# Performance work log

Measured on AMD Instinct MI355X. Metric: run time of the kernel, lower is better.

Reference implementation:

```python
import jax, jax.numpy as jnp
import numpy as np

B, F, D, A = 1024, 33, 128, 128  # batch, num_fields, embed_dim, attn_size (A must equal gnn dim)

def setup_inputs() -> dict:
    key = jax.random.key(0)
    k1, k2, k3, k4 = jax.random.split(key, 4)
    gnn_feature = jax.random.normal(k1, (B, A), dtype=jnp.float32)
    x = jax.random.normal(k2, (B, F, D), dtype=jnp.float32)
    # attention Linear(embed_dim -> attn_size): weight (A, D), bias (A,)
    lim = 1.0 / np.sqrt(D)
    attn_W = jax.random.uniform(k3, (A, D), minval=-lim, maxval=lim, dtype=jnp.float32)
    attn_b = jax.random.uniform(k4, (A,), minval=-lim, maxval=lim, dtype=jnp.float32)
    return {"gnn_feature": gnn_feature, "x": x, "attn_W": attn_W, "attn_b": attn_b}

def reference(gnn_feature, x, attn_W, attn_b):
    num_fields = x.shape[1]
    row, col = np.triu_indices(num_fields, k=1)  # P = F*(F-1)/2 pairs
    inner = x[:, row] * x[:, col]                # [B, P, D]
    fm = jax.nn.relu(jnp.einsum('bpd,ad->bpa', inner, attn_W) + attn_b)  # [B, P, A]
    # bmm(gnn[b,1,A], fm[b,p,A,1]) -> dot product per pair, softmax over pairs
    scores = jnp.einsum('ba,bpa->bp', gnn_feature, fm)  # [B, P]
    attn = jax.nn.softmax(scores, axis=1)               # [B, P]
    attn_output = jnp.einsum('bp,bpd->bd', attn, inner) * 100.0  # [B, D]
    return jnp.concatenate([gnn_feature, attn_output], axis=1)   # [B, A+D]
```

## Files before the change

### kernel.cpp

```cpp
#include <hip/hip_runtime.h>

#define FN 33
#define DN 128
#define AN 128
#define PN 528
#define XS 136
#define TS 36

typedef __attribute__((ext_vector_type(8))) _Float16 half8;
typedef __attribute__((ext_vector_type(4))) float f32x4;
typedef __attribute__((ext_vector_type(4))) unsigned int u32x4;

__device__ __forceinline__ unsigned int pkrtz(float a, float b) {
  return __builtin_bit_cast(unsigned int, __builtin_amdgcn_cvt_pkrtz(a, b));
}

__device__ __forceinline__ float row_sum16(float v) {
  v += __builtin_bit_cast(float, __builtin_amdgcn_update_dpp(0, __builtin_bit_cast(int, v), 0x128, 0xF, 0xF, false));
  v += __builtin_bit_cast(float, __builtin_amdgcn_update_dpp(0, __builtin_bit_cast(int, v), 0x124, 0xF, 0xF, false));
  v += __builtin_bit_cast(float, __builtin_amdgcn_update_dpp(0, __builtin_bit_cast(int, v), 0x122, 0xF, 0xF, false));
  v += __builtin_bit_cast(float, __builtin_amdgcn_update_dpp(0, __builtin_bit_cast(int, v), 0x121, 0xF, 0xF, false));
  return v;
}

__global__ __launch_bounds__(256, 4)
void afm_kernel(const float* __restrict__ gnn, const float* __restrict__ xg,
                const float* __restrict__ Wg,  const float* __restrict__ bg,
                float* __restrict__ out)
{
  __shared__ __align__(16) _Float16 xh[FN * XS];
  __shared__ __align__(16) float attn2d[FN * TS];
  __shared__ __align__(16) float sp[2][PN];
  __shared__ __align__(16) float part[256];
  __shared__ unsigned short rowcol[PN];
  __shared__ float red[8];

  const int tid  = threadIdx.x;
  const int b    = blockIdx.x;
  const int wave = tid >> 6;
  const int lane = tid & 63;
  const int q    = lane >> 4;
  const int u    = lane & 15;
  const int nh   = wave & 1;
  const int mh   = wave >> 1;

  half8 Bf[4][4];
  float garr[4], barr[4];
  #pragma unroll
  for (int nn = 0; nn < 4; nn++) {
    const int a = (nh * 4 + nn) * 16 + u;
    const float* src = Wg + (size_t)a * DN + q * 8;
    #pragma unroll
    for (int kk = 0; kk < 4; kk++) {
      f32x4 w0 = *(const f32x4*)(src + kk * 32);
      f32x4 w1 = *(const f32x4*)(src + kk * 32 + 4);
      u32x4 pk;
      pk.x = pkrtz(w0.x, w0.y);
      pk.y = pkrtz(w0.z, w0.w);
      pk.z = pkrtz(w1.x, w1.y);
      pk.w = pkrtz(w1.z, w1.w);
      Bf[nn][kk] = __builtin_bit_cast(half8, pk);
      asm volatile("" : "+v"(Bf[nn][kk]));
    }
    garr[nn] = gnn[(size_t)b * AN + a];
    barr[nn] = bg[a];
    asm volatile("" : "+v"(garr[nn]), "+v"(barr[nn]));
  }

  for (int idx = tid; idx < FN * TS; idx += 256) attn2d[idx] = 0.0f;

  const f32x4* xg4 = (const f32x4*)(xg + (size_t)b * FN * DN);
  for (int idx = tid; idx < (FN * DN) / 4; idx += 256) {
    f32x4 v = xg4[idx];
    int i  = idx >> 5;
    int d0 = (idx & 31) << 2;
    *(uint2*)&xh[i * XS + d0] = make_uint2(pkrtz(v.x, v.y), pkrtz(v.z, v.w));
  }
  for (int p = tid; p < PN; p += 256) {
    int i = 0, rem = p;
    while (rem >= FN - 1 - i) { rem -= FN - 1 - i; i++; }
    rowcol[p] = (unsigned short)(i | ((i + 1 + rem) << 8));
  }
  __syncthreads();

  const int mt_beg = mh ? 17 : 0;
  const int mt_end = mh ? 33 : 17;
  unsigned int rc_next = rowcol[mt_beg * 16 + u];
  for (int mt = mt_beg; mt < mt_end; ++mt) {
    const unsigned int rc = rc_next;
    if (mt + 1 < mt_end) rc_next = rowcol[(mt + 1) * 16 + u];
    const int r = rc & 255, c = rc >> 8;
    const _Float16* xr_base = &xh[r * XS + q * 8];
    const _Float16* xc_base = &xh[c * XS + q * 8];

    f32x4 acc[4];
    #pragma unroll
    for (int nn = 0; nn < 4; nn++) acc[nn] = (f32x4){0.f, 0.f, 0.f, 0.f};

    #pragma unroll
    for (int kk = 0; kk < 4; kk++) {
      half8 xr = *(const half8*)(xr_base + kk * 32);
      half8 xc = *(const half8*)(xc_base + kk * 32);
      half8 af = xr * xc;
      #pragma unroll
      for (int nn = 0; nn < 4; nn++)
        acc[nn] = __builtin_amdgcn_mfma_f32_16x16x32_f16(af, Bf[nn][kk], acc[nn], 0, 0, 0);
    }

    float sc[4] = {0.f, 0.f, 0.f, 0.f};
    #pragma unroll
    for (int nn = 0; nn < 4; nn++)
      #pragma unroll
      for (int rr = 0; rr < 4; rr++) {
        float fmv = fmaxf(acc[nn][rr] + barr[nn], 0.f);
        sc[rr] = fmaf(fmv, garr[nn], sc[rr]);
      }
    #pragma unroll
    for (int rr = 0; rr < 4; rr++) sc[rr] = row_sum16(sc[rr]);
    if (u == 0)
      *(f32x4*)&sp[nh][mt * 16 + q * 4] = (f32x4){sc[0], sc[1], sc[2], sc[3]};
  }
  __syncthreads();

  float s0 = sp[0][tid] + sp[1][tid];
  float s1 = sp[0][tid + 256] + sp[1][tid + 256];
  float s2 = (tid < 16) ? (sp[0][tid + 512] + sp[1][tid + 512]) : -3.4e38f;
  float m = fmaxf(fmaxf(s0, s1), s2);
  #pragma unroll
  for (int off = 32; off >= 1; off >>= 1) m = fmaxf(m, __shfl_xor(m, off, 64));
  if (lane == 0) red[wave] = m;
  __syncthreads();
  const float smax = fmaxf(fmaxf(red[0], red[1]), fmaxf(red[2], red[3]));

  float e0 = __expf(s0 - smax);
  float e1 = __expf(s1 - smax);
  float e2 = (tid < 16) ? __expf(s2 - smax) : 0.f;
  {
    unsigned int rc = rowcol[tid];
    attn2d[(rc & 255) * TS + ((rc >> 8) - (rc & 255) - 1)] = e0;
    rc = rowcol[tid + 256];
    attn2d[(rc & 255) * TS + ((rc >> 8) - (rc & 255) - 1)] = e1;
    if (tid < 16) {
      rc = rowcol[tid + 512];
      attn2d[(rc & 255) * TS + ((rc >> 8) - (rc & 255) - 1)] = e2;
    }
  }
  float lsum = e0 + e1 + e2;
  #pragma unroll
  for (int off = 32; off >= 1; off >>= 1) lsum += __shfl_xor(lsum, off, 64);
  if (lane == 0) red[4 + wave] = lsum;
  __syncthreads();
  const float Z = red[4] + red[5] + red[6] + red[7];

  {
    const int d = tid & 127;
    const int h = tid >> 7;
    float xcol[36];
    #pragma unroll
    for (int i = 0; i < FN; i++) xcol[i] = (float)xh[i * XS + d];
    xcol[33] = 0.f; xcol[34] = 0.f; xcol[35] = 0.f;

    float acc = 0.f;
    #pragma unroll
    for (int i = 0; i < 32; i++) {
      if ((i & 1) != h) continue;
      const int L = FN - 1 - i;
      const int nf4 = (L + 3) >> 2;
      float ti = 0.f;
      #pragma unroll
      for (int t = 0; t < nf4; t++) {
        f32x4 a4 = *(const f32x4*)&attn2d[i * TS + t * 4];
        ti = fmaf(a4.x, xcol[i + 1 + t * 4 + 0], ti);
        ti = fmaf(a4.y, xcol[i + 1 + t * 4 + 1], ti);
        ti = fmaf(a4.z, xcol[i + 1 + t * 4 + 2], ti);
        ti = fmaf(a4.w, xcol[i + 1 + t * 4 + 3], ti);
      }
      acc = fmaf(xcol[i], ti, acc);
    }
    part[tid] = acc;
  }
  __syncthreads();
  if (tid < DN) {
    float tot = part[tid] + part[tid + 128];
    out[(size_t)b * (AN + DN) + AN + tid] = tot * (100.0f / Z);
  } else {
    const int a = tid - 128;
    out[(size_t)b * (AN + DN) + a] = gnn[(size_t)b * AN + a];
  }
}

extern "C" void kernel_launch(void* const* d_in, const int* in_sizes, int n_in,
                              void* d_out, int out_size, void* d_ws, size_t ws_size,
                              hipStream_t stream) {
  (void)n_in; (void)out_size; (void)d_ws; (void)ws_size;
  const float* gnn  = (const float*)d_in[0];
  const float* x    = (const float*)d_in[1];
  const float* W    = (const float*)d_in[2];
  const float* bias = (const float*)d_in[3];
  float* out = (float*)d_out;
  const int Bn = in_sizes[0] / AN;
  afm_kernel<<<dim3(Bn), dim3(256), 0, stream>>>(gnn, x, W, bias, out);
}
```

Before: 112.6 us.

## Split attention N dimension four ways across waves, each wave covering all pair tiles

```diff
diff --git a/kernel.cpp b/kernel.cpp
--- a/kernel.cpp
+++ b/kernel.cpp
@@ -30,7 +30,7 @@
 {
   __shared__ __align__(16) _Float16 xh[FN * XS];
   __shared__ __align__(16) float attn2d[FN * TS];
-  __shared__ __align__(16) float sp[2][PN];
+  __shared__ __align__(16) float sp[4][PN];
   __shared__ __align__(16) float part[256];
   __shared__ unsigned short rowcol[PN];
   __shared__ float red[8];
@@ -41,14 +41,13 @@
   const int lane = tid & 63;
   const int q    = lane >> 4;
   const int u    = lane & 15;
-  const int nh   = wave & 1;
-  const int mh   = wave >> 1;
-
-  half8 Bf[4][4];
-  float garr[4], barr[4];
+  const int nq   = wave;
+
+  half8 Bf[2][4];
+  float garr[2], barr[2];
   #pragma unroll
-  for (int nn = 0; nn < 4; nn++) {
-    const int a = (nh * 4 + nn) * 16 + u;
+  for (int nn = 0; nn < 2; nn++) {
+    const int a = nq * 32 + nn * 16 + u;
     const float* src = Wg + (size_t)a * DN + q * 8;
     #pragma unroll
     for (int kk = 0; kk < 4; kk++) {
@@ -83,48 +82,93 @@
   }
   __syncthreads();
 
-  const int mt_beg = mh ? 17 : 0;
-  const int mt_end = mh ? 33 : 17;
-  unsigned int rc_next = rowcol[mt_beg * 16 + u];
-  for (int mt = mt_beg; mt < mt_end; ++mt) {
-    const unsigned int rc = rc_next;
-    if (mt + 1 < mt_end) rc_next = rowcol[(mt + 1) * 16 + u];
-    const int r = rc & 255, c = rc >> 8;
-    const _Float16* xr_base = &xh[r * XS + q * 8];
-    const _Float16* xc_base = &xh[c * XS + q * 8];
-
-    f32x4 acc[4];
-    #pragma unroll
-    for (int nn = 0; nn < 4; nn++) acc[nn] = (f32x4){0.f, 0.f, 0.f, 0.f};
-
+  unsigned int rc0 = rowcol[u];
+  unsigned int rc1 = rowcol[16 + u];
+  for (int t = 0; t < 16; ++t) {
+    const int r0 = rc0 & 255, c0 = rc0 >> 8;
+    const int r1 = rc1 & 255, c1 = rc1 >> 8;
+    const _Float16* xr0 = &xh[r0 * XS + q * 8];
+    const _Float16* xc0 = &xh[c0 * XS + q * 8];
+    const _Float16* xr1 = &xh[r1 * XS + q * 8];
+    const _Float16* xc1 = &xh[c1 * XS + q * 8];
+    if (t < 15) {
+      rc0 = rowcol[(t + 1) * 32 + u];
+      rc1 = rowcol[(t + 1) * 32 + 16 + u];
+    } else {
+      rc0 = rowcol[512 + u];
+    }
+
+    f32x4 acc0[2], acc1[2];
+    #pragma unroll
+    for (int nn = 0; nn < 2; nn++) {
+      acc0[nn] = (f32x4){0.f, 0.f, 0.f, 0.f};
+      acc1[nn] = (f32x4){0.f, 0.f, 0.f, 0.f};
+    }
+
+    __builtin_amdgcn_s_setprio(1);
     #pragma unroll
     for (int kk = 0; kk < 4; kk++) {
-      half8 xr = *(const half8*)(xr_base + kk * 32);
-      half8 xc = *(const half8*)(xc_base + kk * 32);
-      half8 af = xr * xc;
-      #pragma unroll
-      for (int nn = 0; nn < 4; nn++)
-        acc[nn] = __builtin_amdgcn_mfma_f32_16x16x32_f16(af, Bf[nn][kk], acc[nn], 0, 0, 0);
-    }
-
-    float sc[4] = {0.f, 0.f, 0.f, 0.f};
-    #pragma unroll
-    for (int nn = 0; nn < 4; nn++)
+      half8 a0 = *(const half8*)(xr0 + kk * 32) * *(const half8*)(xc0 + kk * 32);
+      half8 a1 = *(const half8*)(xr1 + kk * 32) * *(const half8*)(xc1 + kk * 32);
+      acc0[0] = __builtin_amdgcn_mfma_f32_16x16x32_f16(a0, Bf[0][kk], acc0[0], 0, 0, 0);
+      acc1[0] = __builtin_amdgcn_mfma_f32_16x16x32_f16(a1, Bf[0][kk], acc1[0], 0, 0, 0);
+      acc0[1] = __builtin_amdgcn_mfma_f32_16x16x32_f16(a0, Bf[1][kk], acc0[1], 0, 0, 0);
+      acc1[1] = __builtin_amdgcn_mfma_f32_16x16x32_f16(a1, Bf[1][kk], acc1[1], 0, 0, 0);
+    }
+    __builtin_amdgcn_s_setprio(0);
+
+    float sc0[4] = {0.f, 0.f, 0.f, 0.f};
+    float sc1[4] = {0.f, 0.f, 0.f, 0.f};
+    #pragma unroll
+    for (int nn = 0; nn < 2; nn++)
       #pragma unroll
       for (int rr = 0; rr < 4; rr++) {
-        float fmv = fmaxf(acc[nn][rr] + barr[nn], 0.f);
-        sc[rr] = fmaf(fmv, garr[nn], sc[rr]);
+        sc0[rr] = fmaf(fmaxf(acc0[nn][rr] + barr[nn], 0.f), garr[nn], sc0[rr]);
+        sc1[rr] = fmaf(fmaxf(acc1[nn][rr] + barr[nn], 0.f), garr[nn], sc1[rr]);
       }
     #pragma unroll
-    for (int rr = 0; rr < 4; rr++) sc[rr] = row_sum16(sc[rr]);
+    for (int rr = 0; rr < 4; rr++) {
+      sc0[rr] = row_sum16(sc0[rr]);
+      sc1[rr] = row_sum16(sc1[rr]);
+    }
+    if (u == 0) {
+      *(f32x4*)&sp[nq][t * 32 + q * 4]      = (f32x4){sc0[0], sc0[1], sc0[2], sc0[3]};
+      *(f32x4*)&sp[nq][t * 32 + 16 + q * 4] = (f32x4){sc1[0], sc1[1], sc1[2], sc1[3]};
+    }
+  }
+  {
+    const int r0 = rc0 & 255, c0 = rc0 >> 8;
+    const _Float16* xr0 = &xh[r0 * XS + q * 8];
+    const _Float16* xc0 = &xh[c0 * XS + q * 8];
+    f32x4 acc0[2];
+    acc0[0] = (f32x4){0.f, 0.f, 0.f, 0.f};
+    acc0[1] = (f32x4){0.f, 0.f, 0.f, 0.f};
+    __builtin_amdgcn_s_setprio(1);
+    #pragma unroll
+    for (int kk = 0; kk < 4; kk++) {
+      half8 a0 = *(const half8*)(xr0 + kk * 32) * *(const half8*)(xc0 + kk * 32);
+      acc0[0] = __builtin_amdgcn_mfma_f32_16x16x32_f16(a0, Bf[0][kk], acc0[0], 0, 0, 0);
+      acc0[1] = __builtin_amdgcn_mfma_f32_16x16x32_f16(a0, Bf[1][kk], acc0[1], 0, 0, 0);
+    }
+    __builtin_amdgcn_s_setprio(0);
+    float sc0[4] = {0.f, 0.f, 0.f, 0.f};
+    #pragma unroll
+    for (int nn = 0; nn < 2; nn++)
+      #pragma unroll
+      for (int rr = 0; rr < 4; rr++)
+        sc0[rr] = fmaf(fmaxf(acc0[nn][rr] + barr[nn], 0.f), garr[nn], sc0[rr]);
+    #pragma unroll
+    for (int rr = 0; rr < 4; rr++) sc0[rr] = row_sum16(sc0[rr]);
     if (u == 0)
-      *(f32x4*)&sp[nh][mt * 16 + q * 4] = (f32x4){sc[0], sc[1], sc[2], sc[3]};
-  }
-  __syncthreads();
-
-  float s0 = sp[0][tid] + sp[1][tid];
-  float s1 = sp[0][tid + 256] + sp[1][tid + 256];
-  float s2 = (tid < 16) ? (sp[0][tid + 512] + sp[1][tid + 512]) : -3.4e38f;
+      *(f32x4*)&sp[nq][512 + q * 4] = (f32x4){sc0[0], sc0[1], sc0[2], sc0[3]};
+  }
+  __syncthreads();
+
+  float s0 = (sp[0][tid] + sp[1][tid]) + (sp[2][tid] + sp[3][tid]);
+  float s1 = (sp[0][tid + 256] + sp[1][tid + 256]) + (sp[2][tid + 256] + sp[3][tid + 256]);
+  float s2 = (tid < 16)
+           ? ((sp[0][tid + 512] + sp[1][tid + 512]) + (sp[2][tid + 512] + sp[3][tid + 512]))
+           : -3.4e38f;
   float m = fmaxf(fmaxf(s0, s1), s2);
   #pragma unroll
   for (int off = 32; off >= 1; off >>= 1) m = fmaxf(m, __shfl_xor(m, off, 64));
```

New measurement: 110.9 us. Within noise of the previous version (-1.5%).

## Double block size to 512 threads, splitting pair tiles across four wave pairs

Applied to the files above, without the earlier changes.

```diff
diff --git a/kernel.cpp b/kernel.cpp
--- a/kernel.cpp
+++ b/kernel.cpp
@@ -23,7 +23,7 @@
   return v;
 }
 
-__global__ __launch_bounds__(256, 4)
+__global__ __launch_bounds__(512, 4)
 void afm_kernel(const float* __restrict__ gnn, const float* __restrict__ xg,
                 const float* __restrict__ Wg,  const float* __restrict__ bg,
                 float* __restrict__ out)
@@ -31,9 +31,9 @@
   __shared__ __align__(16) _Float16 xh[FN * XS];
   __shared__ __align__(16) float attn2d[FN * TS];
   __shared__ __align__(16) float sp[2][PN];
-  __shared__ __align__(16) float part[256];
+  __shared__ __align__(16) float part[512];
   __shared__ unsigned short rowcol[PN];
-  __shared__ float red[8];
+  __shared__ float red[16];
 
   const int tid  = threadIdx.x;
   const int b    = blockIdx.x;
@@ -42,13 +42,13 @@
   const int q    = lane >> 4;
   const int u    = lane & 15;
   const int nh   = wave & 1;
-  const int mh   = wave >> 1;
+  const int mq   = wave >> 1;
 
   half8 Bf[4][4];
   float garr[4], barr[4];
   #pragma unroll
   for (int nn = 0; nn < 4; nn++) {
-    const int a = (nh * 4 + nn) * 16 + u;
+    const int a = nh * 64 + nn * 16 + u;
     const float* src = Wg + (size_t)a * DN + q * 8;
     #pragma unroll
     for (int kk = 0; kk < 4; kk++) {
@@ -67,28 +67,28 @@
     asm volatile("" : "+v"(garr[nn]), "+v"(barr[nn]));
   }
 
-  for (int idx = tid; idx < FN * TS; idx += 256) attn2d[idx] = 0.0f;
+  for (int idx = tid; idx < FN * TS; idx += 512) attn2d[idx] = 0.0f;
 
   const f32x4* xg4 = (const f32x4*)(xg + (size_t)b * FN * DN);
-  for (int idx = tid; idx < (FN * DN) / 4; idx += 256) {
+  for (int idx = tid; idx < (FN * DN) / 4; idx += 512) {
     f32x4 v = xg4[idx];
     int i  = idx >> 5;
     int d0 = (idx & 31) << 2;
     *(uint2*)&xh[i * XS + d0] = make_uint2(pkrtz(v.x, v.y), pkrtz(v.z, v.w));
   }
-  for (int p = tid; p < PN; p += 256) {
+  for (int p = tid; p < PN; p += 512) {
     int i = 0, rem = p;
     while (rem >= FN - 1 - i) { rem -= FN - 1 - i; i++; }
     rowcol[p] = (unsigned short)(i | ((i + 1 + rem) << 8));
   }
   __syncthreads();
 
-  const int mt_beg = mh ? 17 : 0;
-  const int mt_end = mh ? 33 : 17;
-  unsigned int rc_next = rowcol[mt_beg * 16 + u];
-  for (int mt = mt_beg; mt < mt_end; ++mt) {
+  const int t_beg = (mq == 0) ? 0 : (mq * 8 + 1);
+  const int t_end = (mq + 1) * 8 + 1;
+  unsigned int rc_next = rowcol[t_beg * 16 + u];
+  for (int t = t_beg; t < t_end; ++t) {
     const unsigned int rc = rc_next;
-    if (mt + 1 < mt_end) rc_next = rowcol[(mt + 1) * 16 + u];
+    if (t + 1 < t_end) rc_next = rowcol[(t + 1) * 16 + u];
     const int r = rc & 255, c = rc >> 8;
     const _Float16* xr_base = &xh[r * XS + q * 8];
     const _Float16* xc_base = &xh[c * XS + q * 8];
@@ -97,64 +97,62 @@
     #pragma unroll
     for (int nn = 0; nn < 4; nn++) acc[nn] = (f32x4){0.f, 0.f, 0.f, 0.f};
 
+    __builtin_amdgcn_s_setprio(1);
     #pragma unroll
     for (int kk = 0; kk < 4; kk++) {
-      half8 xr = *(const half8*)(xr_base + kk * 32);
-      half8 xc = *(const half8*)(xc_base + kk * 32);
-      half8 af = xr * xc;
+      half8 af = *(const half8*)(xr_base + kk * 32) * *(const half8*)(xc_base + kk * 32);
       #pragma unroll
       for (int nn = 0; nn < 4; nn++)
         acc[nn] = __builtin_amdgcn_mfma_f32_16x16x32_f16(af, Bf[nn][kk], acc[nn], 0, 0, 0);
     }
+    __builtin_amdgcn_s_setprio(0);
 
     float sc[4] = {0.f, 0.f, 0.f, 0.f};
     #pragma unroll
     for (int nn = 0; nn < 4; nn++)
       #pragma unroll
-      for (int rr = 0; rr < 4; rr++) {
-        float fmv = fmaxf(acc[nn][rr] + barr[nn], 0.f);
-        sc[rr] = fmaf(fmv, garr[nn], sc[rr]);
-      }
+      for (int rr = 0; rr < 4; rr++)
+        sc[rr] = fmaf(fmaxf(acc[nn][rr] + barr[nn], 0.f), garr[nn], sc[rr]);
     #pragma unroll
     for (int rr = 0; rr < 4; rr++) sc[rr] = row_sum16(sc[rr]);
     if (u == 0)
-      *(f32x4*)&sp[nh][mt * 16 + q * 4] = (f32x4){sc[0], sc[1], sc[2], sc[3]};
+      *(f32x4*)&sp[nh][t * 16 + q * 4] = (f32x4){sc[0], sc[1], sc[2], sc[3]};
   }
   __syncthreads();
 
   float s0 = sp[0][tid] + sp[1][tid];
-  float s1 = sp[0][tid + 256] + sp[1][tid + 256];
-  float s2 = (tid < 16) ? (sp[0][tid + 512] + sp[1][tid + 512]) : -3.4e38f;
-  float m = fmaxf(fmaxf(s0, s1), s2);
+  float s1 = (tid < 16) ? (sp[0][tid + 512] + sp[1][tid + 512]) : -3.4e38f;
+  float m = fmaxf(s0, s1);
   #pragma unroll
   for (int off = 32; off >= 1; off >>= 1) m = fmaxf(m, __shfl_xor(m, off, 64));
   if (lane == 0) red[wave] = m;
   __syncthreads();
-  const float smax = fmaxf(fmaxf(red[0], red[1]), fmaxf(red[2], red[3]));
+  float smax = red[0];
+  #pragma unroll
+  for (int w = 1; w < 8; w++) smax = fmaxf(smax, red[w]);
 
   float e0 = __expf(s0 - smax);
-  float e1 = __expf(s1 - smax);
-  float e2 = (tid < 16) ? __expf(s2 - smax) : 0.f;
+  float e1 = (tid < 16) ? __expf(s1 - smax) : 0.f;
   {
     unsigned int rc = rowcol[tid];
     attn2d[(rc & 255) * TS + ((rc >> 8) - (rc & 255) - 1)] = e0;
-    rc = rowcol[tid + 256];
-    attn2d[(rc & 255) * TS + ((rc >> 8) - (rc & 255) - 1)] = e1;
     if (tid < 16) {
       rc = rowcol[tid + 512];
-      attn2d[(rc & 255) * TS + ((rc >> 8) - (rc & 255) - 1)] = e2;
-    }
-  }
-  float lsum = e0 + e1 + e2;
+      attn2d[(rc & 255) * TS + ((rc >> 8) - (rc & 255) - 1)] = e1;
+    }
+  }
+  float lsum = e0 + e1;
   #pragma unroll
   for (int off = 32; off >= 1; off >>= 1) lsum += __shfl_xor(lsum, off, 64);
-  if (lane == 0) red[4 + wave] = lsum;
-  __syncthreads();
-  const float Z = red[4] + red[5] + red[6] + red[7];
+  if (lane == 0) red[8 + wave] = lsum;
+  __syncthreads();
+  float Z = red[8];
+  #pragma unroll
+  for (int w = 1; w < 8; w++) Z += red[8 + w];
 
   {
     const int d = tid & 127;
-    const int h = tid >> 7;
+    const int g = (tid >> 7) & 3;
     float xcol[36];
     #pragma unroll
     for (int i = 0; i < FN; i++) xcol[i] = (float)xh[i * XS + d];
@@ -162,8 +160,8 @@
 
     float acc = 0.f;
     #pragma unroll
-    for (int i = 0; i < 32; i++) {
-      if ((i & 1) != h) continue;
+    for (int i = 0; i < 33; i++) {
+      if ((i & 3) != g) continue;
       const int L = FN - 1 - i;
       const int nf4 = (L + 3) >> 2;
       float ti = 0.f;
@@ -181,9 +179,9 @@
   }
   __syncthreads();
   if (tid < DN) {
-    float tot = part[tid] + part[tid + 128];
+    float tot = (part[tid] + part[tid + 128]) + (part[tid + 256] + part[tid + 384]);
     out[(size_t)b * (AN + DN) + AN + tid] = tot * (100.0f / Z);
-  } else {
+  } else if (tid < 256) {
     const int a = tid - 128;
     out[(size_t)b * (AN + DN) + a] = gnn[(size_t)b * AN + a];
   }
@@ -199,5 +197,5 @@
   const float* bias = (const float*)d_in[3];
   float* out = (float*)d_out;
   const int Bn = in_sizes[0] / AN;
-  afm_kernel<<<dim3(Bn), dim3(256), 0, stream>>>(gnn, x, W, bias, out);
-}
+  afm_kernel<<<dim3(Bn), dim3(512), 0, stream>>>(gnn, x, W, bias, out);
+}
```

After: 121.9 us. +8.2%, slower.

## Process two batch rows per block, overlapping second MFMA walk with first epilogue

Applied to the files above, without the earlier changes.

```diff
diff --git a/kernel.cpp b/kernel.cpp
--- a/kernel.cpp
+++ b/kernel.cpp
@@ -23,20 +23,87 @@
   return v;
 }
 
-__global__ __launch_bounds__(256, 4)
+#define WALK(XHB, GB, SPB)                                                    \
+  {                                                                           \
+    const int t_beg = mh ? 17 : 0;                                            \
+    const int t_end = mh ? 33 : 17;                                           \
+    unsigned int rc_next = rowcol[t_beg * 16 + u];                            \
+    for (int t = t_beg; t < t_end; ++t) {                                     \
+      const unsigned int rc = rc_next;                                        \
+      if (t + 1 < t_end) rc_next = rowcol[(t + 1) * 16 + u];                  \
+      const int r = rc & 255, c = rc >> 8;                                    \
+      const _Float16* xr_base = &XHB[r * XS + q * 8];                         \
+      const _Float16* xc_base = &XHB[c * XS + q * 8];                         \
+      f32x4 acc[4];                                                           \
+      _Pragma("unroll")                                                       \
+      for (int nn = 0; nn < 4; nn++) acc[nn] = (f32x4){0.f, 0.f, 0.f, 0.f};   \
+      __builtin_amdgcn_s_setprio(1);                                          \
+      _Pragma("unroll")                                                       \
+      for (int kk = 0; kk < 4; kk++) {                                        \
+        half8 af = *(const half8*)(xr_base + kk * 32) *                       \
+                   *(const half8*)(xc_base + kk * 32);                        \
+        _Pragma("unroll")                                                     \
+        for (int nn = 0; nn < 4; nn++)                                        \
+          acc[nn] = __builtin_amdgcn_mfma_f32_16x16x32_f16(af, Bf[nn][kk],    \
+                                                           acc[nn], 0, 0, 0);  \
+      }                                                                       \
+      __builtin_amdgcn_s_setprio(0);                                          \
+      float sc[4] = {0.f, 0.f, 0.f, 0.f};                                     \
+      _Pragma("unroll")                                                       \
+      for (int nn = 0; nn < 4; nn++)                                          \
+        _Pragma("unroll")                                                     \
+        for (int rr = 0; rr < 4; rr++)                                        \
+          sc[rr] = fmaf(fmaxf(acc[nn][rr] + barr[nn], 0.f), GB[nn], sc[rr]);  \
+      _Pragma("unroll")                                                       \
+      for (int rr = 0; rr < 4; rr++) sc[rr] = row_sum16(sc[rr]);              \
+      if (u == 0)                                                             \
+        *(f32x4*)&SPB[t * 16 + q * 4] = (f32x4){sc[0], sc[1], sc[2], sc[3]};  \
+    }                                                                         \
+  }
+
+#define EPI(A2D, XHB)                                                         \
+  {                                                                           \
+    const int d = tid & 127;                                                  \
+    const int h = tid >> 7;                                                   \
+    float xcol[36];                                                           \
+    _Pragma("unroll")                                                         \
+    for (int i = 0; i < FN; i++) xcol[i] = (float)XHB[i * XS + d];            \
+    xcol[33] = 0.f; xcol[34] = 0.f; xcol[35] = 0.f;                           \
+    float accv = 0.f;                                                         \
+    _Pragma("unroll")                                                         \
+    for (int i = 0; i < 32; i++) {                                            \
+      if ((i & 1) != h) continue;                                             \
+      const int L = FN - 1 - i;                                               \
+      const int nf4 = (L + 3) >> 2;                                           \
+      float ti = 0.f;                                                         \
+      _Pragma("unroll")                                                       \
+      for (int t = 0; t < nf4; t++) {                                         \
+        f32x4 a4 = *(const f32x4*)&A2D[i * TS + t * 4];                       \
+        ti = fmaf(a4.x, xcol[i + 1 + t * 4 + 0], ti);                         \
+        ti = fmaf(a4.y, xcol[i + 1 + t * 4 + 1], ti);                         \
+        ti = fmaf(a4.z, xcol[i + 1 + t * 4 + 2], ti);                         \
+        ti = fmaf(a4.w, xcol[i + 1 + t * 4 + 3], ti);                         \
+      }                                                                       \
+      accv = fmaf(xcol[i], ti, accv);                                         \
+    }                                                                         \
+    part[tid] = accv;                                                         \
+  }
+
+__global__ __launch_bounds__(256, 2)
 void afm_kernel(const float* __restrict__ gnn, const float* __restrict__ xg,
                 const float* __restrict__ Wg,  const float* __restrict__ bg,
                 float* __restrict__ out)
 {
-  __shared__ __align__(16) _Float16 xh[FN * XS];
-  __shared__ __align__(16) float attn2d[FN * TS];
-  __shared__ __align__(16) float sp[2][PN];
+  __shared__ __align__(16) _Float16 xh[2][FN * XS];
+  __shared__ __align__(16) float attn2d[2][FN * TS];
+  __shared__ __align__(16) float sp[2][2][PN];
   __shared__ __align__(16) float part[256];
   __shared__ unsigned short rowcol[PN];
-  __shared__ float red[8];
+  __shared__ float red[16];
 
   const int tid  = threadIdx.x;
-  const int b    = blockIdx.x;
+  const int b0   = blockIdx.x * 2;
+  const int b1   = b0 + 1;
   const int wave = tid >> 6;
   const int lane = tid & 63;
   const int q    = lane >> 4;
@@ -44,11 +111,21 @@
   const int nh   = wave & 1;
   const int mh   = wave >> 1;
 
+  const f32x4* xb0 = (const f32x4*)(xg + (size_t)b0 * FN * DN);
+  const f32x4* xb1 = (const f32x4*)(xg + (size_t)b1 * FN * DN);
+  f32x4 xv0[4], xv1[4], xt0 = {0,0,0,0}, xt1 = {0,0,0,0};
+  #pragma unroll
+  for (int s = 0; s < 4; s++) xv0[s] = xb0[tid + s * 256];
+  #pragma unroll
+  for (int s = 0; s < 4; s++) xv1[s] = xb1[tid + s * 256];
+  const bool tail = tid < 32;
+  if (tail) { xt0 = xb0[1024 + tid]; xt1 = xb1[1024 + tid]; }
+
   half8 Bf[4][4];
-  float garr[4], barr[4];
+  float g0[4], g1[4], barr[4];
   #pragma unroll
   for (int nn = 0; nn < 4; nn++) {
-    const int a = (nh * 4 + nn) * 16 + u;
+    const int a = nh * 64 + nn * 16 + u;
     const float* src = Wg + (size_t)a * DN + q * 8;
     #pragma unroll
     for (int kk = 0; kk < 4; kk++) {
@@ -62,130 +139,124 @@
       Bf[nn][kk] = __builtin_bit_cast(half8, pk);
       asm volatile("" : "+v"(Bf[nn][kk]));
     }
-    garr[nn] = gnn[(size_t)b * AN + a];
+    g0[nn] = gnn[(size_t)b0 * AN + a];
+    g1[nn] = gnn[(size_t)b1 * AN + a];
     barr[nn] = bg[a];
-    asm volatile("" : "+v"(garr[nn]), "+v"(barr[nn]));
-  }
-
-  for (int idx = tid; idx < FN * TS; idx += 256) attn2d[idx] = 0.0f;
-
-  const f32x4* xg4 = (const f32x4*)(xg + (size_t)b * FN * DN);
-  for (int idx = tid; idx < (FN * DN) / 4; idx += 256) {
-    f32x4 v = xg4[idx];
-    int i  = idx >> 5;
-    int d0 = (idx & 31) << 2;
-    *(uint2*)&xh[i * XS + d0] = make_uint2(pkrtz(v.x, v.y), pkrtz(v.z, v.w));
-  }
-  for (int p = tid; p < PN; p += 256) {
-    int i = 0, rem = p;
-    while (rem >= FN - 1 - i) { rem -= FN - 1 - i; i++; }
-    rowcol[p] = (unsigned short)(i | ((i + 1 + rem) << 8));
-  }
-  __syncthreads();
-
-  const int mt_beg = mh ? 17 : 0;
-  const int mt_end = mh ? 33 : 17;
-  unsigned int rc_next = rowcol[mt_beg * 16 + u];
-  for (int mt = mt_beg; mt < mt_end; ++mt) {
-    const unsigned int rc = rc_next;
-    if (mt + 1 < mt_end) rc_next = rowcol[(mt + 1) * 16 + u];
-    const int r = rc & 255, c = rc >> 8;
-    const _Float16* xr_base = &xh[r * XS + q * 8];
-    const _Float16* xc_base = &xh[c * XS + q * 8];
-
-    f32x4 acc[4];
-    #pragma unroll
-    for (int nn = 0; nn < 4; nn++) acc[nn] = (f32x4){0.f, 0.f, 0.f, 0.f};
-
-    #pragma unroll
-    for (int kk = 0; kk < 4; kk++) {
-      half8 xr = *(const half8*)(xr_base + kk * 32);
-      half8 xc = *(const half8*)(xc_base + kk * 32);
-      half8 af = xr * xc;
-      #pragma unroll
-      for (int nn = 0; nn < 4; nn++)
-        acc[nn] = __builtin_amdgcn_mfma_f32_16x16x32_f16(af, Bf[nn][kk], acc[nn], 0, 0, 0);
-    }
-
-    float sc[4] = {0.f, 0.f, 0.f, 0.f};
-    #pragma unroll
-    for (int nn = 0; nn < 4; nn++)
-      #pragma unroll
-      for (int rr = 0; rr < 4; rr++) {
-        float fmv = fmaxf(acc[nn][rr] + barr[nn], 0.f);
-        sc[rr] = fmaf(fmv, garr[nn], sc[rr]);
-      }
-    #pragma unroll
-    for (int rr = 0; rr < 4; rr++) sc[rr] = row_sum16(sc[rr]);
-    if (u == 0)
-      *(f32x4*)&sp[nh][mt * 16 + q * 4] = (f32x4){sc[0], sc[1], sc[2], sc[3]};
-  }
-  __syncthreads();
-
-  float s0 = sp[0][tid] + sp[1][tid];
-  float s1 = sp[0][tid + 256] + sp[1][tid + 256];
-  float s2 = (tid < 16) ? (sp[0][tid + 512] + sp[1][tid + 512]) : -3.4e38f;
-  float m = fmaxf(fmaxf(s0, s1), s2);
-  #pragma unroll
-  for (int off = 32; off >= 1; off >>= 1) m = fmaxf(m, __shfl_xor(m, off, 64));
-  if (lane == 0) red[wave] = m;
-  __syncthreads();
-  const float smax = fmaxf(fmaxf(red[0], red[1]), fmaxf(red[2], red[3]));
-
-  float e0 = __expf(s0 - smax);
-  float e1 = __expf(s1 - smax);
-  float e2 = (tid < 16) ? __expf(s2 - smax) : 0.f;
-  {
+    asm volatile("" : "+v"(g0[nn]), "+v"(g1[nn]), "+v"(barr[nn]));
+  }
+
+  {
+    float* a2z = &attn2d[0][0];
+    for (int idx = tid; idx < 2 * FN * TS; idx += 256) a2z[idx] = 0.0f;
+    for (int p = tid; p < PN; p += 256) {
+      int i = 0, rem = p;
+      while (rem >= FN - 1 - i) { rem -= FN - 1 - i; i++; }
+      rowcol[p] = (unsigned short)(i | ((i + 1 + rem) << 8));
+    }
+  }
+
+  #pragma unroll
+  for (int s = 0; s < 4; s++) {
+    const int idx = tid + s * 256;
+    const int i = idx >> 5, d0 = (idx & 31) << 2;
+    *(uint2*)&xh[0][i * XS + d0] = make_uint2(pkrtz(xv0[s].x, xv0[s].y), pkrtz(xv0[s].z, xv0[s].w));
+    *(uint2*)&xh[1][i * XS + d0] = make_uint2(pkrtz(xv1[s].x, xv1[s].y), pkrtz(xv1[s].z, xv1[s].w));
+  }
+  if (tail) {
+    const int idx = 1024 + tid;
+    const int i = idx >> 5, d0 = (idx & 31) << 2;
+    *(uint2*)&xh[0][i * XS + d0] = make_uint2(pkrtz(xt0.x, xt0.y), pkrtz(xt0.z, xt0.w));
+    *(uint2*)&xh[1][i * XS + d0] = make_uint2(pkrtz(xt1.x, xt1.y), pkrtz(xt1.z, xt1.w));
+  }
+  __syncthreads();
+
+  WALK(xh[0], g0, (&sp[0][nh][0]));
+  __syncthreads();
+
+  float s0a = sp[0][0][tid] + sp[0][1][tid];
+  float s1a = sp[0][0][tid + 256] + sp[0][1][tid + 256];
+  float s2a = (tid < 16) ? (sp[0][0][tid + 512] + sp[0][1][tid + 512]) : -3.4e38f;
+  {
+    float m = fmaxf(fmaxf(s0a, s1a), s2a);
+    #pragma unroll
+    for (int off = 32; off >= 1; off >>= 1) m = fmaxf(m, __shfl_xor(m, off, 64));
+    if (lane == 0) red[wave] = m;
+  }
+  __syncthreads();
+
+  const float smax0 = fmaxf(fmaxf(red[0], red[1]), fmaxf(red[2], red[3]));
+  {
+    float e0 = __expf(s0a - smax0);
+    float e1 = __expf(s1a - smax0);
+    float e2 = (tid < 16) ? __expf(s2a - smax0) : 0.f;
     unsigned int rc = rowcol[tid];
-    attn2d[(rc & 255) * TS + ((rc >> 8) - (rc & 255) - 1)] = e0;
+    attn2d[0][(rc & 255) * TS + ((rc >> 8) - (rc & 255) - 1)] = e0;
     rc = rowcol[tid + 256];
-    attn2d[(rc & 255) * TS + ((rc >> 8) - (rc & 255) - 1)] = e1;
+    attn2d[0][(rc & 255) * TS + ((rc >> 8) - (rc & 255) - 1)] = e1;
     if (tid < 16) {
       rc = rowcol[tid + 512];
-      attn2d[(rc & 255) * TS + ((rc >> 8) - (rc & 255) - 1)] = e2;
-    }
-  }
-  float lsum = e0 + e1 + e2;
-  #pragma unroll
-  for (int off = 32; off >= 1; off >>= 1) lsum += __shfl_xor(lsum, off, 64);
-  if (lane == 0) red[4 + wave] = lsum;
-  __syncthreads();
-  const float Z = red[4] + red[5] + red[6] + red[7];
-
-  {
-    const int d = tid & 127;
-    const int h = tid >> 7;
-    float xcol[36];
-    #pragma unroll
-    for (int i = 0; i < FN; i++) xcol[i] = (float)xh[i * XS + d];
-    xcol[33] = 0.f; xcol[34] = 0.f; xcol[35] = 0.f;
-
-    float acc = 0.f;
-    #pragma unroll
-    for (int i = 0; i < 32; i++) {
-      if ((i & 1) != h) continue;
-      const int L = FN - 1 - i;
-      const int nf4 = (L + 3) >> 2;
-      float ti = 0.f;
-      #pragma unroll
-      for (int t = 0; t < nf4; t++) {
-        f32x4 a4 = *(const f32x4*)&attn2d[i * TS + t * 4];
-        ti = fmaf(a4.x, xcol[i + 1 + t * 4 + 0], ti);
-        ti = fmaf(a4.y, xcol[i + 1 + t * 4 + 1], ti);
-        ti = fmaf(a4.z, xcol[i + 1 + t * 4 + 2], ti);
-        ti = fmaf(a4.w, xcol[i + 1 + t * 4 + 3], ti);
-      }
-      acc = fmaf(xcol[i], ti, acc);
-    }
-    part[tid] = acc;
-  }
-  __syncthreads();
+      attn2d[0][(rc & 255) * TS + ((rc >> 8) - (rc & 255) - 1)] = e2;
+    }
+    float lsum = e0 + e1 + e2;
+    #pragma unroll
+    for (int off = 32; off >= 1; off >>= 1) lsum += __shfl_xor(lsum, off, 64);
+    if (lane == 0) red[4 + wave] = lsum;
+  }
+  __syncthreads();
+  const float Z0 = (red[4] + red[5]) + (red[6] + red[7]);
+
+  WALK(xh[1], g1, (&sp[1][nh][0]));
+  EPI(attn2d[0], xh[0]);
+  __syncthreads();
+
+  float s0b = sp[1][0][tid] + sp[1][1][tid];
+  float s1b = sp[1][0][tid + 256] + sp[1][1][tid + 256];
+  float s2b = (tid < 16) ? (sp[1][0][tid + 512] + sp[1][1][tid + 512]) : -3.4e38f;
+  {
+    float m = fmaxf(fmaxf(s0b, s1b), s2b);
+    #pragma unroll
+    for (int off = 32; off >= 1; off >>= 1) m = fmaxf(m, __shfl_xor(m, off, 64));
+    if (lane == 0) red[8 + wave] = m;
+  }
   if (tid < DN) {
     float tot = part[tid] + part[tid + 128];
-    out[(size_t)b * (AN + DN) + AN + tid] = tot * (100.0f / Z);
+    out[(size_t)b0 * (AN + DN) + AN + tid] = tot * (100.0f / Z0);
   } else {
     const int a = tid - 128;
-    out[(size_t)b * (AN + DN) + a] = gnn[(size_t)b * AN + a];
+    out[(size_t)b0 * (AN + DN) + a] = gnn[(size_t)b0 * AN + a];
+  }
+  __syncthreads();
+
+  const float smax1 = fmaxf(fmaxf(red[8], red[9]), fmaxf(red[10], red[11]));
+  {
+    float e0 = __expf(s0b - smax1);
+    float e1 = __expf(s1b - smax1);
+    float e2 = (tid < 16) ? __expf(s2b - smax1) : 0.f;
+    unsigned int rc = rowcol[tid];
+    attn2d[1][(rc & 255) * TS + ((rc >> 8) - (rc & 255) - 1)] = e0;
+    rc = rowcol[tid + 256];
+    attn2d[1][(rc & 255) * TS + ((rc >> 8) - (rc & 255) - 1)] = e1;
+    if (tid < 16) {
+      rc = rowcol[tid + 512];
+      attn2d[1][(rc & 255) * TS + ((rc >> 8) - (rc & 255) - 1)] = e2;
+    }
+    float lsum = e0 + e1 + e2;
+    #pragma unroll
+    for (int off = 32; off >= 1; off >>= 1) lsum += __shfl_xor(lsum, off, 64);
+    if (lane == 0) red[12 + wave] = lsum;
+  }
+  __syncthreads();
+  const float Z1 = (red[12] + red[13]) + (red[14] + red[15]);
+
+  EPI(attn2d[1], xh[1]);
+  __syncthreads();
+
+  if (tid < DN) {
+    float tot = part[tid] + part[tid + 128];
+    out[(size_t)b1 * (AN + DN) + AN + tid] = tot * (100.0f / Z1);
+  } else {
+    const int a = tid - 128;
+    out[(size_t)b1 * (AN + DN) + a] = gnn[(size_t)b1 * AN + a];
   }
 }
 
@@ -199,5 +270,5 @@
   const float* bias = (const float*)d_in[3];
   float* out = (float*)d_out;
   const int Bn = in_sizes[0] / AN;
-  afm_kernel<<<dim3(Bn), dim3(256), 0, stream>>>(gnn, x, W, bias, out);
-}
+  afm_kernel<<<dim3(Bn / 2), dim3(256), 0, stream>>>(gnn, x, W, bias, out);
+}
```

Result: faster. 106.9 us (-5.1%).
